# Kernel tuning notes

Hardware: AMD Instinct MI355X
Metric: run time of the kernel (lower is better)

Reference implementation:

```python
import jax, jax.numpy as jnp
import numpy as np

N = 100000   # nodes
E = 1600000  # edges
F_IN = 256   # input features
H = 128      # hidden
C = 40       # classes


def setup_inputs() -> dict:
    key = jax.random.key(0)
    ks = jax.random.split(key, 6)
    x = jax.random.normal(ks[0], (N, F_IN), dtype=jnp.float32)
    edge_index = jax.random.randint(ks[1], (2, E), 0, N, dtype=jnp.int32)
    edge_attr = jax.random.uniform(ks[2], (E,), dtype=jnp.float32)
    # Glorot-style init like GCNConv
    W1 = jax.random.normal(ks[3], (F_IN, H), dtype=jnp.float32) * (1.0 / np.sqrt(F_IN))
    b1 = jnp.zeros((H,), dtype=jnp.float32)
    W2 = jax.random.normal(ks[4], (H, C), dtype=jnp.float32) * (1.0 / np.sqrt(H))
    b2 = jnp.zeros((C,), dtype=jnp.float32)
    return {"x": x, "edge_index": edge_index, "edge_attr": edge_attr,
            "W1": W1, "b1": b1, "W2": W2, "b2": b2}


def _gcn_norm(edge_index, edge_weight, num_nodes):
    # PyG gcn_norm: add self-loops (weight 1), symmetric D^{-1/2} A D^{-1/2}
    row, col = edge_index[0], edge_index[1]
    loop = jnp.arange(num_nodes, dtype=row.dtype)
    row = jnp.concatenate([row, loop])
    col = jnp.concatenate([col, loop])
    ew = jnp.concatenate([edge_weight, jnp.ones((num_nodes,), edge_weight.dtype)])
    deg = jax.ops.segment_sum(ew, col, num_segments=num_nodes)
    dinv = jnp.where(deg > 0, jax.lax.rsqrt(deg), 0.0)
    norm = dinv[row] * ew * dinv[col]
    return row, col, norm


def _gcn_conv(x, row, col, norm, W, b):
    h = x @ W                              # [N, out] dense transform first
    msg = h[row] * norm[:, None]           # gather source + edge scaling
    out = jax.ops.segment_sum(msg, col, num_segments=x.shape[0])  # scatter-add
    return out + b


def reference(x, edge_index, edge_attr, W1, b1, W2, b2):
    row, col, norm = _gcn_norm(edge_index, edge_attr, x.shape[0])
    h = _gcn_conv(x, row, col, norm, W1, b1)
    h = jax.nn.relu(h)
    # dropout is identity in eval mode
    h = _gcn_conv(h, row, col, norm, W2, b2)
    return jax.nn.log_softmax(h, axis=1)
```

## Files before the change

kernel.cpp:

```cpp
#include <hip/hip_runtime.h>

#define N_NODES 100000
#define N_EDGES 1600000
#define F_INPUT 256
#define H_DIM   128
#define C_DIM   40
#define NB1     ((N_NODES + 255) / 256)

typedef short  bf8   __attribute__((ext_vector_type(8)));
typedef float  f32x4 __attribute__((ext_vector_type(4)));
typedef float  f32x2 __attribute__((ext_vector_type(2)));
typedef unsigned short u16x8 __attribute__((ext_vector_type(8)));

static __device__ __forceinline__ unsigned short f2bf(float f) {
    union { float f; unsigned u; } v; v.f = f;
    unsigned r = v.u + 0x7FFFu + ((v.u >> 16) & 1u);
    return (unsigned short)(r >> 16);
}
static __device__ __forceinline__ float bf2f(unsigned short b) {
    union { unsigned u; float f; } v; v.u = ((unsigned)b) << 16;
    return v.f;
}
static __device__ __forceinline__ f32x2 bfpair(unsigned u) {
    union { unsigned u; float f; } lo, hi;
    lo.u = u << 16; hi.u = u & 0xFFFF0000u;
    return (f32x2){lo.f, hi.f};
}

__global__ void k_init(unsigned* packed) {
    int i = blockIdx.x * 256 + threadIdx.x;
    if (i < N_NODES) packed[i] = (1u << 16);
}

__global__ void k_count(const int* __restrict__ col, const float* __restrict__ ea,
                        unsigned* packed, int* __restrict__ rank) {
    int e = blockIdx.x * 256 + threadIdx.x;
    if (e < N_EDGES) {
        int c = col[e];
        unsigned q = __float2uint_rn(ea[e] * 65536.0f);
        unsigned old = atomicAdd(packed + c, (1u << 24) | q);
        rank[e] = (int)(old >> 24);
    }
}

__global__ void k_scan1(const unsigned* __restrict__ packed, int* start, int* bsum,
                        float* dinv) {
    __shared__ int s[256];
    int i = blockIdx.x * 256 + threadIdx.x;
    unsigned pk = (i < N_NODES) ? packed[i] : 0;
    if (i < N_NODES) dinv[i] = rsqrtf((float)(pk & 0xFFFFFFu) * (1.0f / 65536.0f));
    int v = (int)(pk >> 24);
    s[threadIdx.x] = v; __syncthreads();
    for (int off = 1; off < 256; off <<= 1) {
        int t = (threadIdx.x >= off) ? s[threadIdx.x - off] : 0;
        __syncthreads();
        s[threadIdx.x] += t;
        __syncthreads();
    }
    if (i < N_NODES) start[i] = s[threadIdx.x] - v;
    if (threadIdx.x == 255) bsum[blockIdx.x] = s[255];
}

__global__ void k_scan2(int* bsum) {
    __shared__ int s[512];
    int v = (threadIdx.x < NB1) ? bsum[threadIdx.x] : 0;
    s[threadIdx.x] = v; __syncthreads();
    for (int off = 1; off < 512; off <<= 1) {
        int t = (threadIdx.x >= off) ? s[threadIdx.x - off] : 0;
        __syncthreads();
        s[threadIdx.x] += t;
        __syncthreads();
    }
    if (threadIdx.x < NB1) bsum[threadIdx.x] = s[threadIdx.x] - v;
}

__global__ void k_scatter(const int* __restrict__ row, const int* __restrict__ col,
                          const float* __restrict__ ea,
                          const int* __restrict__ start, const int* __restrict__ bsum,
                          const int* __restrict__ rank, int2* __restrict__ csr) {
    int e = blockIdx.x * 256 + threadIdx.x;
    if (e < N_EDGES) {
        int c = col[e];
        int pos = start[c] + bsum[c >> 8] + rank[e];
        csr[pos] = make_int2(row[e], __float_as_int(ea[e]));
    }
}

__global__ void k_packW(const float* __restrict__ W1, const float* __restrict__ W2,
                        unsigned short* Wp1, unsigned short* Wp2) {
    int idx = blockIdx.x * 256 + threadIdx.x;
    if (idx < 32768) {
        int j = idx & 7, lane = (idx >> 3) & 63, ks = (idx >> 9) & 7, nt = idx >> 12;
        int m = lane & 15, q = lane >> 4;
        int k = ks * 32 + q * 8 + j;
        int n = nt * 16 + m;
        Wp1[idx] = f2bf(W1[k * H_DIM + n]);
    }
    int idx2 = idx - 32768;
    if (idx2 >= 0 && idx2 < 6144) {
        int j = idx2 & 7, lane = (idx2 >> 3) & 63, ks = (idx2 >> 9) & 3, nt = idx2 >> 11;
        int m = lane & 15, q = lane >> 4;
        int k = ks * 32 + q * 8 + j;
        int n = nt * 16 + m;
        Wp2[idx2] = (n < C_DIM) ? f2bf(W2[k * C_DIM + n]) : (unsigned short)0;
    }
}

__global__ __launch_bounds__(256, 4) void k_gemm1(const float* __restrict__ x,
                        const unsigned short* __restrict__ Wp,
                        const float* __restrict__ dinv, unsigned short* __restrict__ h) {
    __shared__ unsigned short lds_out[64 * H_DIM];
    int tid = threadIdx.x;
    int wave = tid >> 6, lane = tid & 63;
    int m = lane & 15, q = lane >> 4;
    int row0 = blockIdx.x * 64 + wave * 16;
    int rowA = row0 + m; if (rowA >= N_NODES) rowA = N_NODES - 1;

    f32x4 acc[8];
#pragma unroll
    for (int i = 0; i < 8; i++) acc[i] = (f32x4){0.f, 0.f, 0.f, 0.f};
    const float* xr = x + (long)rowA * F_INPUT + q * 8;
#pragma unroll
    for (int ks = 0; ks < 8; ks++) {
        float4 a0 = *(const float4*)(xr + ks * 32);
        float4 a1 = *(const float4*)(xr + ks * 32 + 4);
        bf8 a;
        a[0] = (short)f2bf(a0.x); a[1] = (short)f2bf(a0.y);
        a[2] = (short)f2bf(a0.z); a[3] = (short)f2bf(a0.w);
        a[4] = (short)f2bf(a1.x); a[5] = (short)f2bf(a1.y);
        a[6] = (short)f2bf(a1.z); a[7] = (short)f2bf(a1.w);
#pragma unroll
        for (int nt = 0; nt < 8; nt++) {
            bf8 b = *(const bf8*)(Wp + (((nt * 8 + ks) * 64 + lane) << 3));
            acc[nt] = __builtin_amdgcn_mfma_f32_16x16x32_bf16(a, b, acc[nt], 0, 0, 0);
        }
    }
    int orow = row0 + q * 4;
    f32x4 dr;
    if (orow + 3 < N_NODES) dr = *(const f32x4*)(dinv + orow);
    else {
#pragma unroll
        for (int r = 0; r < 4; r++) {
            int rr = orow + r; if (rr >= N_NODES) rr = N_NODES - 1;
            dr[r] = dinv[rr];
        }
    }
    int lrow = wave * 16 + q * 4;
#pragma unroll
    for (int nt = 0; nt < 8; nt++)
#pragma unroll
        for (int r = 0; r < 4; r++)
            lds_out[(lrow + r) * H_DIM + nt * 16 + m] = f2bf(acc[nt][r] * dr[r]);
    __syncthreads();
    int valid = N_NODES - blockIdx.x * 64; if (valid > 64) valid = 64;
    unsigned short* gbase = h + (size_t)blockIdx.x * 64 * H_DIM;
#pragma unroll
    for (int i = 0; i < 4; i++) {
        int idx = (i * 256 + tid) * 8;
        if (idx < valid * H_DIM)
            *(u16x8*)(gbase + idx) = *(const u16x8*)(lds_out + idx);
    }
}

__global__ void k_agg1(const unsigned short* __restrict__ h, const int2* __restrict__ csr,
                       const int* __restrict__ start, const int* __restrict__ bsum,
                       const unsigned* __restrict__ packed,
                       const float* __restrict__ dinv, const float* __restrict__ b1,
                       unsigned short* __restrict__ h1) {
    int c = (blockIdx.x * blockDim.x + threadIdx.x) >> 6;
    int lane = threadIdx.x & 63;
    if (c >= N_NODES) return;
    int eg = lane >> 4, cl = lane & 15;
    float di = dinv[c];
    int s = start[c] + bsum[c >> 8];
    int n = (int)(packed[c] >> 24);

    float w[5]; int r[5];
#pragma unroll
    for (int t = 0; t < 5; t++) {
        int i = eg + 4 * t;
        int2 p = csr[s + ((i < n) ? i : 0)];
        bool val = (i < n);
        r[t] = val ? p.x : c;
        w[t] = val ? __int_as_float(p.y) : 0.f;
    }
    uint4 gv[5];
#pragma unroll
    for (int t = 0; t < 5; t++)
        gv[t] = *(const uint4*)(h + (long)r[t] * H_DIM + cl * 8);
    uint4 selfv = (eg == 0) ? *(const uint4*)(h + (long)c * H_DIM + cl * 8)
                            : (uint4){0, 0, 0, 0};

    f32x2 acc[4];
#pragma unroll
    for (int k = 0; k < 4; k++) acc[k] = (f32x2){0.f, 0.f};
    {
        unsigned sv[4] = {selfv.x, selfv.y, selfv.z, selfv.w};
        if (eg == 0)
#pragma unroll
            for (int k = 0; k < 4; k++) acc[k] += bfpair(sv[k]);
    }
#pragma unroll
    for (int t = 0; t < 5; t++) {
        unsigned vv[4] = {gv[t].x, gv[t].y, gv[t].z, gv[t].w};
        f32x2 ww = (f32x2){w[t], w[t]};
#pragma unroll
        for (int k = 0; k < 4; k++) acc[k] += ww * bfpair(vv[k]);
    }
    for (int i = 20 + eg; i < n; i += 4) {
        int2 p = csr[s + i];
        uint4 v4 = *(const uint4*)(h + (long)p.x * H_DIM + cl * 8);
        unsigned vv[4] = {v4.x, v4.y, v4.z, v4.w};
        float wt = __int_as_float(p.y);
        f32x2 ww = (f32x2){wt, wt};
#pragma unroll
        for (int k = 0; k < 4; k++) acc[k] += ww * bfpair(vv[k]);
    }
#pragma unroll
    for (int k = 0; k < 4; k++) {
        acc[k].x += __shfl_xor(acc[k].x, 16); acc[k].y += __shfl_xor(acc[k].y, 16);
        acc[k].x += __shfl_xor(acc[k].x, 32); acc[k].y += __shfl_xor(acc[k].y, 32);
    }
    if (eg == 0) {
        u16x8 o;
#pragma unroll
        for (int k = 0; k < 4; k++) {
            o[2 * k]     = f2bf(fmaxf(di * acc[k].x + b1[cl * 8 + 2 * k], 0.f));
            o[2 * k + 1] = f2bf(fmaxf(di * acc[k].y + b1[cl * 8 + 2 * k + 1], 0.f));
        }
        *(u16x8*)(h1 + (long)c * H_DIM + cl * 8) = o;
    }
}

__global__ __launch_bounds__(256, 4) void k_gemm2(const unsigned short* __restrict__ h1,
                        const unsigned short* __restrict__ Wp,
                        const float* __restrict__ dinv, unsigned short* __restrict__ h2) {
    __shared__ unsigned short lds_out[64 * C_DIM];
    int tid = threadIdx.x;
    int wave = tid >> 6, lane = tid & 63;
    int m = lane & 15, q = lane >> 4;
    int row0 = blockIdx.x * 64 + wave * 16;
    int rowA = row0 + m; if (rowA >= N_NODES) rowA = N_NODES - 1;

    f32x4 acc[3];
#pragma unroll
    for (int i = 0; i < 3; i++) acc[i] = (f32x4){0.f, 0.f, 0.f, 0.f};
    const unsigned short* hr = h1 + (long)rowA * H_DIM + q * 8;
#pragma unroll
    for (int ks = 0; ks < 4; ks++) {
        bf8 a = *(const bf8*)(hr + ks * 32);
#pragma unroll
        for (int nt = 0; nt < 3; nt++) {
            bf8 b = *(const bf8*)(Wp + (((nt * 4 + ks) * 64 + lane) << 3));
            acc[nt] = __builtin_amdgcn_mfma_f32_16x16x32_bf16(a, b, acc[nt], 0, 0, 0);
        }
    }
    int orow = row0 + q * 4;
    f32x4 dr;
    if (orow + 3 < N_NODES) dr = *(const f32x4*)(dinv + orow);
    else {
#pragma unroll
        for (int r = 0; r < 4; r++) {
            int rr = orow + r; if (rr >= N_NODES) rr = N_NODES - 1;
            dr[r] = dinv[rr];
        }
    }
    int lrow = wave * 16 + q * 4;
#pragma unroll
    for (int nt = 0; nt < 3; nt++)
#pragma unroll
        for (int r = 0; r < 4; r++) {
            int colo = nt * 16 + m;
            if (colo < C_DIM)
                lds_out[(lrow + r) * C_DIM + colo] = f2bf(acc[nt][r] * dr[r]);
        }
    __syncthreads();
    int valid = N_NODES - blockIdx.x * 64; if (valid > 64) valid = 64;
    unsigned short* gbase = h2 + (size_t)blockIdx.x * 64 * C_DIM;
    int total = valid * C_DIM;
#pragma unroll
    for (int i = 0; i < 3; i++) {
        int idx = (i * 256 + tid) * 4;
        if (idx < total)
            *(uint2*)(gbase + idx) = *(const uint2*)(lds_out + idx);
    }
}

__global__ void k_agg2(const unsigned short* __restrict__ h2, const int2* __restrict__ csr,
                       const int* __restrict__ start, const int* __restrict__ bsum,
                       const unsigned* __restrict__ packed,
                       const float* __restrict__ dinv, const float* __restrict__ b2,
                       float* __restrict__ out) {
    int c = (blockIdx.x * blockDim.x + threadIdx.x) >> 6;
    int lane = threadIdx.x & 63;
    if (c >= N_NODES) return;
    int eg = lane >> 3, cl = lane & 7;
    float di = dinv[c];
    int s = start[c] + bsum[c >> 8];
    int n = (int)(packed[c] >> 24);

    float w[3]; int r[3];
#pragma unroll
    for (int t = 0; t < 3; t++) {
        int i = eg + 8 * t;
        int2 p = csr[s + ((i < n) ? i : 0)];
        bool val = (i < n);
        r[t] = val ? p.x : c;
        w[t] = val ? __int_as_float(p.y) : 0.f;
    }
    uint4 gv[3] = {{0,0,0,0},{0,0,0,0},{0,0,0,0}};
    uint4 selfv = {0, 0, 0, 0};
    if (cl < 5) {
#pragma unroll
        for (int t = 0; t < 3; t++)
            gv[t] = *(const uint4*)(h2 + (long)r[t] * C_DIM + cl * 8);
        if (eg == 0) selfv = *(const uint4*)(h2 + (long)c * C_DIM + cl * 8);
    }
    f32x2 acc[4];
#pragma unroll
    for (int k = 0; k < 4; k++) acc[k] = (f32x2){0.f, 0.f};
    {
        unsigned sv[4] = {selfv.x, selfv.y, selfv.z, selfv.w};
        if (eg == 0 && cl < 5)
#pragma unroll
            for (int k = 0; k < 4; k++) acc[k] += bfpair(sv[k]);
    }
#pragma unroll
    for (int t = 0; t < 3; t++) {
        unsigned vv[4] = {gv[t].x, gv[t].y, gv[t].z, gv[t].w};
        f32x2 ww = (f32x2){w[t], w[t]};
#pragma unroll
        for (int k = 0; k < 4; k++) acc[k] += ww * bfpair(vv[k]);
    }
    for (int i = 24 + eg; i < n; i += 8) {
        int2 p = csr[s + i];
        if (cl < 5) {
            uint4 v4 = *(const uint4*)(h2 + (long)p.x * C_DIM + cl * 8);
            unsigned vv[4] = {v4.x, v4.y, v4.z, v4.w};
            float wt = __int_as_float(p.y);
            f32x2 ww = (f32x2){wt, wt};
#pragma unroll
            for (int k = 0; k < 4; k++) acc[k] += ww * bfpair(vv[k]);
        }
    }
#pragma unroll
    for (int k = 0; k < 4; k++) {
        acc[k].x += __shfl_xor(acc[k].x, 8);  acc[k].y += __shfl_xor(acc[k].y, 8);
        acc[k].x += __shfl_xor(acc[k].x, 16); acc[k].y += __shfl_xor(acc[k].y, 16);
        acc[k].x += __shfl_xor(acc[k].x, 32); acc[k].y += __shfl_xor(acc[k].y, 32);
    }
    float v[8];
    float lm = -INFINITY;
    if (cl < 5) {
#pragma unroll
        for (int k = 0; k < 4; k++) {
            v[2 * k]     = di * acc[k].x + b2[cl * 8 + 2 * k];
            v[2 * k + 1] = di * acc[k].y + b2[cl * 8 + 2 * k + 1];
            lm = fmaxf(lm, fmaxf(v[2 * k], v[2 * k + 1]));
        }
    }
    lm = fmaxf(lm, __shfl_xor(lm, 1));
    lm = fmaxf(lm, __shfl_xor(lm, 2));
    lm = fmaxf(lm, __shfl_xor(lm, 4));
    float ls = 0.f;
    if (cl < 5) {
#pragma unroll
        for (int j = 0; j < 8; j++) ls += __expf(v[j] - lm);
    }
    ls += __shfl_xor(ls, 1);
    ls += __shfl_xor(ls, 2);
    ls += __shfl_xor(ls, 4);
    if (eg == 0 && cl < 5) {
        float lsm = lm + logf(ls);
        f32x4 o0, o1;
#pragma unroll
        for (int j = 0; j < 4; j++) { o0[j] = v[j] - lsm; o1[j] = v[j + 4] - lsm; }
        *(f32x4*)(out + (long)c * C_DIM + cl * 8)     = o0;
        *(f32x4*)(out + (long)c * C_DIM + cl * 8 + 4) = o1;
    }
}

extern "C" void kernel_launch(void* const* d_in, const int* in_sizes, int n_in,
                              void* d_out, int out_size, void* d_ws, size_t ws_size,
                              hipStream_t stream) {
    const float* x  = (const float*)d_in[0];
    const int*   ei = (const int*)d_in[1];
    const float* ea = (const float*)d_in[2];
    const float* W1 = (const float*)d_in[3];
    const float* b1 = (const float*)d_in[4];
    const float* W2 = (const float*)d_in[5];
    const float* b2 = (const float*)d_in[6];
    const int* row = ei;
    const int* col = ei + N_EDGES;

    char* ws = (char*)d_ws;
    size_t off = 0;
    auto alloc = [&](size_t bytes) -> void* {
        void* p = ws + off;
        off = (off + bytes + 255) & ~(size_t)255;
        return p;
    };
    unsigned*       packed = (unsigned*)alloc((size_t)N_NODES * 4);
    float*          dinv   = (float*)alloc((size_t)N_NODES * 4);
    int*            rank   = (int*)alloc((size_t)N_EDGES * 4);
    int*            start  = (int*)alloc((size_t)N_NODES * 4);
    int*            bsum   = (int*)alloc(512 * 4);
    int2*           csr    = (int2*)alloc((size_t)N_EDGES * 8);
    unsigned short* Wp1    = (unsigned short*)alloc(32768 * 2);
    unsigned short* Wp2    = (unsigned short*)alloc(6144 * 2);
    unsigned short* h      = (unsigned short*)alloc((size_t)(N_NODES + 64) * H_DIM * 2);
    unsigned short* h1     = (unsigned short*)alloc((size_t)N_NODES * H_DIM * 2);
    unsigned short* h2     = (unsigned short*)alloc((size_t)(N_NODES + 64) * C_DIM * 2);

    k_init<<<NB1, 256, 0, stream>>>(packed);
    k_count<<<N_EDGES / 256, 256, 0, stream>>>(col, ea, packed, rank);
    k_scan1<<<NB1, 256, 0, stream>>>(packed, start, bsum, dinv);
    k_scan2<<<1, 512, 0, stream>>>(bsum);
    k_scatter<<<N_EDGES / 256, 256, 0, stream>>>(row, col, ea, start, bsum, rank, csr);
    k_packW<<<153, 256, 0, stream>>>(W1, W2, Wp1, Wp2);
    k_gemm1<<<(N_NODES + 63) / 64, 256, 0, stream>>>(x, Wp1, dinv, h);
    k_agg1<<<N_NODES / 4, 256, 0, stream>>>(h, csr, start, bsum, packed, dinv, b1, h1);
    k_gemm2<<<(N_NODES + 63) / 64, 256, 0, stream>>>(h1, Wp2, dinv, h2);
    k_agg2<<<N_NODES / 4, 256, 0, stream>>>(h2, csr, start, bsum, packed, dinv, b2, (float*)d_out);
}
```

Measured before the change: 431.6 us.

## Fuse degree counting with GEMM1 and fold source normalization into CSR weights

The source-side dinv scaling moves out of both GEMM epilogues and into the CSR edge weights (ea*dinv[row]). The self-loop term in the aggregations is scaled by dinv explicitly instead. With that dependency gone, GEMM1 no longer needs dinv, so it is interleaved with the atomic degree-count kernel in one launch (every fifth block does GEMM work), letting the compute-bound GEMM overlap the atomic-bound counting. Init and weight packing are merged into one prologue kernel, which cuts launch count. The risk is interference between the GEMM and atomic blocks and a slight change in rounding, since h is stored unscaled in bf16.

```diff
diff --git a/kernel.cpp b/kernel.cpp
--- a/kernel.cpp
+++ b/kernel.cpp
@@ -6,6 +6,9 @@
 #define H_DIM   128
 #define C_DIM   40
 #define NB1     ((N_NODES + 255) / 256)
+#define NGEMM1  1563
+#define NCOUNT  6250
+#define NMEGA   (NGEMM1 + NCOUNT)
 
 typedef short  bf8   __attribute__((ext_vector_type(8)));
 typedef float  f32x4 __attribute__((ext_vector_type(4)));
@@ -27,19 +30,88 @@
     return (f32x2){lo.f, hi.f};
 }
 
-__global__ void k_init(unsigned* packed) {
-    int i = blockIdx.x * 256 + threadIdx.x;
-    if (i < N_NODES) packed[i] = (1u << 16);
-}
-
-__global__ void k_count(const int* __restrict__ col, const float* __restrict__ ea,
-                        unsigned* packed, int* __restrict__ rank) {
-    int e = blockIdx.x * 256 + threadIdx.x;
-    if (e < N_EDGES) {
-        int c = col[e];
-        unsigned q = __float2uint_rn(ea[e] * 65536.0f);
-        unsigned old = atomicAdd(packed + c, (1u << 24) | q);
-        rank[e] = (int)(old >> 24);
+__global__ void k_pre(unsigned* packed, const float* __restrict__ W1,
+                      const float* __restrict__ W2,
+                      unsigned short* Wp1, unsigned short* Wp2) {
+    if (blockIdx.x < NB1) {
+        int i = blockIdx.x * 256 + threadIdx.x;
+        if (i < N_NODES) packed[i] = (1u << 16);
+        return;
+    }
+    int idx = (blockIdx.x - NB1) * 256 + threadIdx.x;
+    if (idx < 32768) {
+        int j = idx & 7, lane = (idx >> 3) & 63, ks = (idx >> 9) & 7, nt = idx >> 12;
+        int m = lane & 15, q = lane >> 4;
+        Wp1[idx] = f2bf(W1[(ks * 32 + q * 8 + j) * H_DIM + nt * 16 + m]);
+    }
+    int idx2 = idx - 32768;
+    if (idx2 >= 0 && idx2 < 6144) {
+        int j = idx2 & 7, lane = (idx2 >> 3) & 63, ks = (idx2 >> 9) & 3, nt = idx2 >> 11;
+        int m = lane & 15, q = lane >> 4;
+        int n = nt * 16 + m;
+        Wp2[idx2] = (n < C_DIM) ? f2bf(W2[(ks * 32 + q * 8 + j) * C_DIM + n]) : (unsigned short)0;
+    }
+}
+
+__global__ __launch_bounds__(256, 4) void k_mega(
+        const float* __restrict__ x, const unsigned short* __restrict__ Wp,
+        unsigned short* __restrict__ h,
+        const int* __restrict__ col, const float* __restrict__ ea,
+        unsigned* packed, int* __restrict__ rank) {
+    __shared__ unsigned short lds_out[64 * H_DIM];
+    int b = blockIdx.x;
+    bool is_gemm = (b % 5 == 0);
+    if (!is_gemm) {
+        int cb = b - b / 5 - 1;
+        int e = cb * 256 + threadIdx.x;
+        if (e < N_EDGES) {
+            int c = col[e];
+            unsigned q = __float2uint_rn(ea[e] * 65536.0f);
+            unsigned old = atomicAdd(packed + c, (1u << 24) | q);
+            rank[e] = (int)(old >> 24);
+        }
+        return;
+    }
+    int tile = b / 5;
+    int tid = threadIdx.x;
+    int wave = tid >> 6, lane = tid & 63;
+    int m = lane & 15, q = lane >> 4;
+    int row0 = tile * 64 + wave * 16;
+    int rowA = row0 + m; if (rowA >= N_NODES) rowA = N_NODES - 1;
+
+    f32x4 acc[8];
+#pragma unroll
+    for (int i = 0; i < 8; i++) acc[i] = (f32x4){0.f, 0.f, 0.f, 0.f};
+    const float* xr = x + (long)rowA * F_INPUT + q * 8;
+#pragma unroll
+    for (int ks = 0; ks < 8; ks++) {
+        float4 a0 = *(const float4*)(xr + ks * 32);
+        float4 a1 = *(const float4*)(xr + ks * 32 + 4);
+        bf8 a;
+        a[0] = (short)f2bf(a0.x); a[1] = (short)f2bf(a0.y);
+        a[2] = (short)f2bf(a0.z); a[3] = (short)f2bf(a0.w);
+        a[4] = (short)f2bf(a1.x); a[5] = (short)f2bf(a1.y);
+        a[6] = (short)f2bf(a1.z); a[7] = (short)f2bf(a1.w);
+#pragma unroll
+        for (int nt = 0; nt < 8; nt++) {
+            bf8 bb = *(const bf8*)(Wp + (((nt * 8 + ks) * 64 + lane) << 3));
+            acc[nt] = __builtin_amdgcn_mfma_f32_16x16x32_bf16(a, bb, acc[nt], 0, 0, 0);
+        }
+    }
+    int lrow = wave * 16 + q * 4;
+#pragma unroll
+    for (int nt = 0; nt < 8; nt++)
+#pragma unroll
+        for (int r = 0; r < 4; r++)
+            lds_out[(lrow + r) * H_DIM + nt * 16 + m] = f2bf(acc[nt][r]);
+    __syncthreads();
+    int valid = N_NODES - tile * 64; if (valid > 64) valid = 64;
+    unsigned short* gbase = h + (size_t)tile * 64 * H_DIM;
+#pragma unroll
+    for (int i = 0; i < 4; i++) {
+        int idx = (i * 256 + tid) * 8;
+        if (idx < valid * H_DIM)
+            *(u16x8*)(gbase + idx) = *(const u16x8*)(lds_out + idx);
     }
 }
 
@@ -75,90 +147,16 @@
 }
 
 __global__ void k_scatter(const int* __restrict__ row, const int* __restrict__ col,
-                          const float* __restrict__ ea,
+                          const float* __restrict__ ea, const float* __restrict__ dinv,
                           const int* __restrict__ start, const int* __restrict__ bsum,
                           const int* __restrict__ rank, int2* __restrict__ csr) {
     int e = blockIdx.x * 256 + threadIdx.x;
     if (e < N_EDGES) {
         int c = col[e];
+        int r = row[e];
         int pos = start[c] + bsum[c >> 8] + rank[e];
-        csr[pos] = make_int2(row[e], __float_as_int(ea[e]));
-    }
-}
-
-__global__ void k_packW(const float* __restrict__ W1, const float* __restrict__ W2,
-                        unsigned short* Wp1, unsigned short* Wp2) {
-    int idx = blockIdx.x * 256 + threadIdx.x;
-    if (idx < 32768) {
-        int j = idx & 7, lane = (idx >> 3) & 63, ks = (idx >> 9) & 7, nt = idx >> 12;
-        int m = lane & 15, q = lane >> 4;
-        int k = ks * 32 + q * 8 + j;
-        int n = nt * 16 + m;
-        Wp1[idx] = f2bf(W1[k * H_DIM + n]);
-    }
-    int idx2 = idx - 32768;
-    if (idx2 >= 0 && idx2 < 6144) {
-        int j = idx2 & 7, lane = (idx2 >> 3) & 63, ks = (idx2 >> 9) & 3, nt = idx2 >> 11;
-        int m = lane & 15, q = lane >> 4;
-        int k = ks * 32 + q * 8 + j;
-        int n = nt * 16 + m;
-        Wp2[idx2] = (n < C_DIM) ? f2bf(W2[k * C_DIM + n]) : (unsigned short)0;
-    }
-}
-
-__global__ __launch_bounds__(256, 4) void k_gemm1(const float* __restrict__ x,
-                        const unsigned short* __restrict__ Wp,
-                        const float* __restrict__ dinv, unsigned short* __restrict__ h) {
-    __shared__ unsigned short lds_out[64 * H_DIM];
-    int tid = threadIdx.x;
-    int wave = tid >> 6, lane = tid & 63;
-    int m = lane & 15, q = lane >> 4;
-    int row0 = blockIdx.x * 64 + wave * 16;
-    int rowA = row0 + m; if (rowA >= N_NODES) rowA = N_NODES - 1;
-
-    f32x4 acc[8];
-#pragma unroll
-    for (int i = 0; i < 8; i++) acc[i] = (f32x4){0.f, 0.f, 0.f, 0.f};
-    const float* xr = x + (long)rowA * F_INPUT + q * 8;
-#pragma unroll
-    for (int ks = 0; ks < 8; ks++) {
-        float4 a0 = *(const float4*)(xr + ks * 32);
-        float4 a1 = *(const float4*)(xr + ks * 32 + 4);
-        bf8 a;
-        a[0] = (short)f2bf(a0.x); a[1] = (short)f2bf(a0.y);
-        a[2] = (short)f2bf(a0.z); a[3] = (short)f2bf(a0.w);
-        a[4] = (short)f2bf(a1.x); a[5] = (short)f2bf(a1.y);
-        a[6] = (short)f2bf(a1.z); a[7] = (short)f2bf(a1.w);
-#pragma unroll
-        for (int nt = 0; nt < 8; nt++) {
-            bf8 b = *(const bf8*)(Wp + (((nt * 8 + ks) * 64 + lane) << 3));
-            acc[nt] = __builtin_amdgcn_mfma_f32_16x16x32_bf16(a, b, acc[nt], 0, 0, 0);
-        }
-    }
-    int orow = row0 + q * 4;
-    f32x4 dr;
-    if (orow + 3 < N_NODES) dr = *(const f32x4*)(dinv + orow);
-    else {
-#pragma unroll
-        for (int r = 0; r < 4; r++) {
-            int rr = orow + r; if (rr >= N_NODES) rr = N_NODES - 1;
-            dr[r] = dinv[rr];
-        }
-    }
-    int lrow = wave * 16 + q * 4;
-#pragma unroll
-    for (int nt = 0; nt < 8; nt++)
-#pragma unroll
-        for (int r = 0; r < 4; r++)
-            lds_out[(lrow + r) * H_DIM + nt * 16 + m] = f2bf(acc[nt][r] * dr[r]);
-    __syncthreads();
-    int valid = N_NODES - blockIdx.x * 64; if (valid > 64) valid = 64;
-    unsigned short* gbase = h + (size_t)blockIdx.x * 64 * H_DIM;
-#pragma unroll
-    for (int i = 0; i < 4; i++) {
-        int idx = (i * 256 + tid) * 8;
-        if (idx < valid * H_DIM)
-            *(u16x8*)(gbase + idx) = *(const u16x8*)(lds_out + idx);
+        float w = ea[e] * dinv[r];
+        csr[pos] = make_int2(r, __float_as_int(w));
     }
 }
 
@@ -196,9 +194,10 @@
     for (int k = 0; k < 4; k++) acc[k] = (f32x2){0.f, 0.f};
     {
         unsigned sv[4] = {selfv.x, selfv.y, selfv.z, selfv.w};
+        f32x2 dd = (f32x2){di, di};
         if (eg == 0)
 #pragma unroll
-            for (int k = 0; k < 4; k++) acc[k] += bfpair(sv[k]);
+            for (int k = 0; k < 4; k++) acc[k] += dd * bfpair(sv[k]);
     }
 #pragma unroll
     for (int t = 0; t < 5; t++) {
@@ -234,7 +233,7 @@
 
 __global__ __launch_bounds__(256, 4) void k_gemm2(const unsigned short* __restrict__ h1,
                         const unsigned short* __restrict__ Wp,
-                        const float* __restrict__ dinv, unsigned short* __restrict__ h2) {
+                        unsigned short* __restrict__ h2) {
     __shared__ unsigned short lds_out[64 * C_DIM];
     int tid = threadIdx.x;
     int wave = tid >> 6, lane = tid & 63;
@@ -255,16 +254,6 @@
             acc[nt] = __builtin_amdgcn_mfma_f32_16x16x32_bf16(a, b, acc[nt], 0, 0, 0);
         }
     }
-    int orow = row0 + q * 4;
-    f32x4 dr;
-    if (orow + 3 < N_NODES) dr = *(const f32x4*)(dinv + orow);
-    else {
-#pragma unroll
-        for (int r = 0; r < 4; r++) {
-            int rr = orow + r; if (rr >= N_NODES) rr = N_NODES - 1;
-            dr[r] = dinv[rr];
-        }
-    }
     int lrow = wave * 16 + q * 4;
 #pragma unroll
     for (int nt = 0; nt < 3; nt++)
@@ -272,7 +261,7 @@
         for (int r = 0; r < 4; r++) {
             int colo = nt * 16 + m;
             if (colo < C_DIM)
-                lds_out[(lrow + r) * C_DIM + colo] = f2bf(acc[nt][r] * dr[r]);
+                lds_out[(lrow + r) * C_DIM + colo] = f2bf(acc[nt][r]);
         }
     __syncthreads();
     int valid = N_NODES - blockIdx.x * 64; if (valid > 64) valid = 64;
@@ -321,9 +310,10 @@
     for (int k = 0; k < 4; k++) acc[k] = (f32x2){0.f, 0.f};
     {
         unsigned sv[4] = {selfv.x, selfv.y, selfv.z, selfv.w};
+        f32x2 dd = (f32x2){di, di};
         if (eg == 0 && cl < 5)
 #pragma unroll
-            for (int k = 0; k < 4; k++) acc[k] += bfpair(sv[k]);
+            for (int k = 0; k < 4; k++) acc[k] += dd * bfpair(sv[k]);
     }
 #pragma unroll
     for (int t = 0; t < 3; t++) {
@@ -412,14 +402,12 @@
     unsigned short* h1     = (unsigned short*)alloc((size_t)N_NODES * H_DIM * 2);
     unsigned short* h2     = (unsigned short*)alloc((size_t)(N_NODES + 64) * C_DIM * 2);
 
-    k_init<<<NB1, 256, 0, stream>>>(packed);
-    k_count<<<N_EDGES / 256, 256, 0, stream>>>(col, ea, packed, rank);
+    k_pre<<<NB1 + 152, 256, 0, stream>>>(packed, W1, W2, Wp1, Wp2);
+    k_mega<<<NMEGA, 256, 0, stream>>>(x, Wp1, h, col, ea, packed, rank);
     k_scan1<<<NB1, 256, 0, stream>>>(packed, start, bsum, dinv);
     k_scan2<<<1, 512, 0, stream>>>(bsum);
-    k_scatter<<<N_EDGES / 256, 256, 0, stream>>>(row, col, ea, start, bsum, rank, csr);
-    k_packW<<<153, 256, 0, stream>>>(W1, W2, Wp1, Wp2);
-    k_gemm1<<<(N_NODES + 63) / 64, 256, 0, stream>>>(x, Wp1, dinv, h);
+    k_scatter<<<N_EDGES / 256, 256, 0, stream>>>(row, col, ea, dinv, start, bsum, rank, csr);
     k_agg1<<<N_NODES / 4, 256, 0, stream>>>(h, csr, start, bsum, packed, dinv, b1, h1);
-    k_gemm2<<<(N_NODES + 63) / 64, 256, 0, stream>>>(h1, Wp2, dinv, h2);
+    k_gemm2<<<(N_NODES + 63) / 64, 256, 0, stream>>>(h1, Wp2, h2);
     k_agg2<<<N_NODES / 4, 256, 0, stream>>>(h2, csr, start, bsum, packed, dinv, b2, (float*)d_out);
 }
```

New measurement: 403.5 us. 6.5% less time.
